# Kernel optimization log

Measured on AMD Instinct MI355X. Metric: run time of the kernel, lower is better.

## Reference

```python
import jax, jax.numpy as jnp
import numpy as np

LN_EPS = 1e-5


def conv2d(x, w, b, stride, pad):
    # x: NCHW, w: OIHW
    y = jax.lax.conv_general_dilated(
        x, w, (stride, stride), [(pad, pad), (pad, pad)],
        dimension_numbers=("NCHW", "OIHW", "NCHW"))
    return y + b[None, :, None, None]


def gdn(x, gamma, beta):
    # y_c = x_c / sqrt(beta_c + sum_j gamma_cj * x_j^2)  (1x1 conv on x^2)
    norm = jnp.einsum("bchw,dc->bdhw", x * x, gamma) + beta[None, :, None, None]
    return x / jnp.sqrt(norm)


def layernorm(x, w, b):
    mu = jnp.mean(x, axis=-1, keepdims=True)
    var = jnp.var(x, axis=-1, keepdims=True)
    return (x - mu) / jnp.sqrt(var + LN_EPS) * w + b


def setup_inputs() -> dict:
    key = jax.random.key(0)
    ks = jax.random.split(key, 16)
    r = lambda i, shape: (jax.random.normal(ks[i], shape) * 0.02).astype(jnp.float32)
    N, M, K, D = 128, 192, 192, 128
    return {
        "x_p": jax.random.normal(ks[0], (4, 16, 3, 64, 64), jnp.float32),
        "y_g": jax.random.normal(ks[1], (64, K, 32), jnp.float32),
        "conv1_w": r(2, (N, 3, 5, 5)), "conv1_b": jnp.zeros((N,), jnp.float32),
        "gamma1": (0.1 * jnp.eye(N) + 1e-3).astype(jnp.float32), "beta1": jnp.ones((N,), jnp.float32),
        "conv2_w": r(3, (N, N, 5, 5)), "conv2_b": jnp.zeros((N,), jnp.float32),
        "gamma2": (0.1 * jnp.eye(N) + 1e-3).astype(jnp.float32), "beta2": jnp.ones((N,), jnp.float32),
        "conv3_w": r(4, (M, N, 3, 3)), "conv3_b": jnp.zeros((M,), jnp.float32),
        "ln_q_w": jnp.ones((M,), jnp.float32), "ln_q_b": jnp.zeros((M,), jnp.float32),
        "ln_kv_w": jnp.ones((K,), jnp.float32), "ln_kv_b": jnp.zeros((K,), jnp.float32),
        "ln_out_w": jnp.ones((M,), jnp.float32), "ln_out_b": jnp.zeros((M,), jnp.float32),
        "Wq": r(5, (D, M)), "Wk": r(6, (D, K)), "v_w": r(7, (1, D)),
        "Wv": r(8, (M, K)), "out_w": r(9, (M, M)), "out_b": jnp.zeros((M,), jnp.float32),
    }


def reference(x_p, y_g, conv1_w, conv1_b, gamma1, beta1, conv2_w, conv2_b,
              gamma2, beta2, conv3_w, conv3_b, ln_q_w, ln_q_b, ln_kv_w, ln_kv_b,
              ln_out_w, ln_out_b, Wq, Wk, v_w, Wv, out_w, out_b):
    B, P, C, Hp, Wp = x_p.shape
    x = x_p.reshape(B * P, C, Hp, Wp)
    # local encoder: conv s2 -> GDN -> conv s2 -> GDN -> conv s1 k3
    x = gdn(conv2d(x, conv1_w, conv1_b, 2, 2), gamma1, beta1)
    x = gdn(conv2d(x, conv2_w, conv2_b, 2, 2), gamma2, beta2)
    y_local = conv2d(x, conv3_w, conv3_b, 1, 1)          # (BP, M, h, w)
    BP, M, h, w = y_local.shape
    q = y_local.reshape(BP, M, h * w).transpose(0, 2, 1)  # (BP, Tq, M)
    kv = y_g.reshape(BP, y_g.shape[1], -1).transpose(0, 2, 1)  # (BP, Tk, K)
    q = layernorm(q, ln_q_w, ln_q_b)
    kv = layernorm(kv, ln_kv_w, ln_kv_b)
    # Bahdanau additive attention
    q_proj = jnp.einsum("bqm,dm->bqd", q, Wq)            # (BP, Tq, D)
    k_proj = jnp.einsum("bkc,dc->bkd", kv, Wk)           # (BP, Tk, D)
    energy = jnp.einsum("bqkd,d->bqk",
                        jnp.tanh(q_proj[:, :, None, :] + k_proj[:, None, :, :]),
                        v_w[0])                           # (BP, Tq, Tk)
    alpha = jax.nn.softmax(energy, axis=-1)
    v_proj = jnp.einsum("bkc,mc->bkm", kv, Wv)           # (BP, Tk, M)
    context = jnp.einsum("bqk,bkm->bqm", alpha, v_proj)
    context = jnp.einsum("bqm,nm->bqn", context, out_w) + out_b
    fused = layernorm(q + context, ln_out_w, ln_out_b)
    return fused.transpose(0, 2, 1).reshape(BP, M, h, w)
```

## Files before the change

kernel.cpp:

```cpp
#include <hip/hip_runtime.h>
#include <cstddef>
#include <cstdint>


typedef __bf16 bf16x8 __attribute__((ext_vector_type(8)));
typedef float floatx4 __attribute__((ext_vector_type(4)));
typedef unsigned short ushortT;
typedef unsigned short ushort8v __attribute__((ext_vector_type(8)));

#if __has_builtin(__builtin_amdgcn_exp2f)
#define EXP2F(x) __builtin_amdgcn_exp2f(x)
#else
#define EXP2F(x) exp2f(x)
#endif
#if __has_builtin(__builtin_amdgcn_rcpf)
#define RCPF(x) __builtin_amdgcn_rcpf(x)
#else
#define RCPF(x) (1.f / (x))
#endif

__device__ __forceinline__ ushortT f2bf(float f) {
  unsigned u = __builtin_bit_cast(unsigned, f);
  unsigned r = (u + 0x7FFFu + ((u >> 16) & 1u)) >> 16;
  return (ushortT)r;
}
__device__ __forceinline__ float bf2f(ushortT u) {
  return __builtin_bit_cast(float, ((unsigned)u) << 16);
}

static constexpr size_t OFF_X2BF = 4194304;
static constexpr size_t OFF_X3BF = 9437184;
static constexpr size_t OFF_QRAW = 10485760;
static constexpr size_t OFF_WBQ  = 21299200;
static constexpr size_t OFF_WBK  = 21311488;
static constexpr size_t OFF_WBV  = 21323776;
static constexpr size_t OFF_WBO  = 21342208;
static constexpr size_t OFF_WT2  = 26079232;
static constexpr size_t OFF_WT3  = 26284032;
static constexpr size_t OFF_WC1  = 26394624;
static constexpr size_t OFF_GB1  = 26406912;
static constexpr size_t OFF_GB2  = 26415104;
static constexpr size_t OFF_KP   = 0;
static constexpr size_t OFF_VT   = 262144;

__device__ __constant__ int d_TWI2[4][9] = {{ 0, 2, 4,10,12,14,20,22,24},
                                            { 1, 3,11,13,21,23, 0, 0, 0},
                                            { 5, 7, 9,15,17,19, 0, 0, 0},
                                            { 6, 8,16,18, 0, 0, 0, 0, 0}};
__device__ __constant__ int d_NT2[4] = {9, 6, 6, 4};

__device__ void dev_convw3(const float* w, ushortT* wt, int mode, int total,
                           int idx) {
  if (idx >= total) return;
  int j    = idx & 7;
  int om   = (idx >> 3) & 63;
  int kg   = (idx >> 9) & 3;
  int slab = idx >> 11;
  int mt, s, tap, T;
  if (mode == 0) {
    int ph;
    if (slab < 72) ph = 0; else if (slab < 120) ph = 1;
    else if (slab < 168) ph = 2; else ph = 3;
    const int st[4] = {0, 72, 120, 168};
    const int ns[4] = {36, 24, 24, 16};
    int rel = slab - st[ph];
    mt = rel / ns[ph]; s = rel % ns[ph];
    tap = d_TWI2[ph][s >> 2]; T = 25;
  } else {
    mt = slab / 36; s = slab % 36; tap = s >> 2; T = 9;
  }
  int cc = s & 3;
  int c  = cc * 32 + kg * 8 + j;
  int oc = mt * 64 + om;
  wt[idx] = f2bf(w[(size_t)(oc * 128 + c) * T + tap]);
}

__device__ void dev_convw1(const float* w, ushortT* wt, int idx) {
  if (idx >= 20480) return;
  int k    = idx & 31;
  int oc   = (idx >> 5) & 127;
  int slab = idx >> 12;
  int ph, i;
  if (slab < 2) { ph = 0; i = slab; } else { ph = slab - 1; i = 0; }
  int kg = k >> 3, jj = k & 7;
  int tidx = i * 8 + jj;
  float val = 0.f;
  if (kg < 3 && tidx < d_NT2[ph]) {
    int tap = d_TWI2[ph][tidx];
    val = w[(size_t)(oc * 3 + kg) * 25 + tap];
  }
  wt[idx] = f2bf(val);
}

__device__ void dev_wcast(const float* w, ushortT* wb, int total, float scale,
                          int idx) {
  if (idx < total) wb[idx] = f2bf(w[idx] * scale);
}

__global__ __launch_bounds__(256) void prep_kernel(
    const float* __restrict__ conv2_w, ushortT* __restrict__ wt2,
    const float* __restrict__ conv3_w, ushortT* __restrict__ wt3,
    const float* __restrict__ conv1_w, ushortT* __restrict__ wc1,
    const float* __restrict__ Wq, ushortT* __restrict__ wbq,
    const float* __restrict__ Wk, ushortT* __restrict__ wbk,
    const float* __restrict__ Wv, ushortT* __restrict__ wbv,
    const float* __restrict__ out_w, ushortT* __restrict__ wbo,
    const float* __restrict__ gamma1, ushortT* __restrict__ gb1,
    const float* __restrict__ gamma2, ushortT* __restrict__ gb2) {
  constexpr float C2LE = 2.88539008177792681f;
  int blk = blockIdx.x, tid = threadIdx.x;
  if (blk < 1600)      dev_convw3(conv2_w, wt2, 0, 409600, blk * 256 + tid);
  else if (blk < 2464) dev_convw3(conv3_w, wt3, 1, 221184, (blk - 1600) * 256 + tid);
  else if (blk < 2544) dev_convw1(conv1_w, wc1, (blk - 2464) * 256 + tid);
  else if (blk < 2640) dev_wcast(Wq, wbq, 24576, C2LE, (blk - 2544) * 256 + tid);
  else if (blk < 2736) dev_wcast(Wk, wbk, 24576, C2LE, (blk - 2640) * 256 + tid);
  else if (blk < 2880) dev_wcast(Wv, wbv, 36864, 1.f, (blk - 2736) * 256 + tid);
  else if (blk < 3024) dev_wcast(out_w, wbo, 36864, 1.f, (blk - 2880) * 256 + tid);
  else if (blk < 3088) dev_wcast(gamma1, gb1, 16384, 1.f, (blk - 3024) * 256 + tid);
  else                 dev_wcast(gamma2, gb2, 16384, 1.f, (blk - 3088) * 256 + tid);
}

__global__ __launch_bounds__(256, 1) void conv1_gdn_kernel(
    const float* __restrict__ x, const ushortT* __restrict__ wc1,
    const float* __restrict__ bias, const ushortT* __restrict__ gb1,
    const float* __restrict__ beta1, ushortT* __restrict__ outb) {
  int b  = blockIdx.x >> 2;
  int yg = blockIdx.x & 3;
  int y0 = yg * 8;

  int wave = threadIdx.x >> 6;
  int lane = threadIdx.x & 63;
  int ln15 = lane & 15;
  int kg   = lane >> 4;
  int tid  = threadIdx.x;

  __shared__ ushortT smem[30280];
  ushortT* simg = smem;
  ushortT* sA   = smem + 4680;

  for (int j = tid; j < 2340; j += 256) ((unsigned*)simg)[j] = 0u;
  __syncthreads();

  int ihBase = 2 * y0 - 2;
  const float* xb = x + (size_t)b * 3 * 4096;
  for (int j = tid; j < 960; j += 256) {
    int q = j & 15;
    int rr = j >> 4;
    int c = rr / 20, ihl = rr % 20;
    int ih = ihBase + ihl;
    if (ih >= 0 && ih < 64) {
      float4 v = *(const float4*)&xb[c * 4096 + ih * 64 + q * 4];
      int pr = ih & 1, u = ih >> 1;
      int lr = u - y0 + 1;
      int base0 = ((pr * 2 + 0) * 3 + c) * 360 + lr * 36;
      int base1 = ((pr * 2 + 1) * 3 + c) * 360 + lr * 36;
      simg[base0 + 2 * q + 1] = f2bf(v.x);
      simg[base1 + 2 * q + 1] = f2bf(v.y);
      simg[base0 + 2 * q + 2] = f2bf(v.z);
      simg[base1 + 2 * q + 2] = f2bf(v.w);
    }
  }
  for (int j = tid; j < 2560; j += 256) {
    int chunk = j & 3, row = j >> 2;
    uint4 v = *(const uint4*)&wc1[row * 32 + chunk * 8];
    *(uint4*)&sA[row * 40 + chunk * 8] = v;
  }
  __syncthreads();

  constexpr int TDR[4][9] = {{-1,-1,-1, 0, 0, 0, 1, 1, 1},
                             {-1,-1, 0, 0, 1, 1, 0, 0, 0},
                             {-1,-1,-1, 0, 0, 0, 0, 0, 0},
                             {-1,-1, 0, 0, 0, 0, 0, 0, 0}};
  constexpr int TDC[4][9] = {{-1, 0, 1,-1, 0, 1,-1, 0, 1},
                             {-1, 0,-1, 0,-1, 0, 0, 0, 0},
                             {-1, 0, 1,-1, 0, 1, 0, 0, 0},
                             {-1, 0,-1, 0, 0, 0, 0, 0, 0}};
  constexpr int NT[4]  = {9, 6, 6, 4};
  constexpr int NM[4]  = {2, 1, 1, 1};
  constexpr int SB[4]  = {0, 2, 3, 4};

  ushort8v Bf[4][5];
  #pragma unroll
  for (int ntl = 0; ntl < 4; ++ntl) {
    int ntg = wave * 4 + ntl;
    int yloc = ntg >> 1;
    int xx = (ntg & 1) * 16 + ln15;
    int lbase = (yloc + 1) * 36 + xx + 1 + kg * 360;
    #pragma unroll
    for (int ph = 0; ph < 4; ++ph) {
      int pbase = ph * 1080 + lbase;
      #pragma unroll
      for (int i = 0; i < 2; ++i) {
        if (i < NM[ph]) {
          ushort8v bv;
          #pragma unroll
          for (int j = 0; j < 8; ++j) {
            int tidx = i * 8 + j;
            if (tidx >= NT[ph]) tidx = 0;
            int off = TDR[ph][tidx] * 36 + TDC[ph][tidx];
            bv[j] = simg[pbase + off];
          }
          Bf[ntl][SB[ph] + i] = bv;
        }
      }
    }
  }

  ushort4 xq[8][4];
  #pragma unroll
  for (int m = 0; m < 8; ++m) {
    bf16x8 Af[5];
    #pragma unroll
    for (int s = 0; s < 5; ++s)
      Af[s] = *(const bf16x8*)&sA[(s * 128 + m * 16 + ln15) * 40 + kg * 8];
    int oc0 = m * 16 + kg * 4;
    float4 bv = *(const float4*)&bias[oc0];
    #pragma unroll
    for (int ntl = 0; ntl < 4; ++ntl) {
      floatx4 acc = (floatx4)0.f;
      #pragma unroll
      for (int s = 0; s < 5; ++s)
        acc = __builtin_amdgcn_mfma_f32_16x16x32_bf16(
            Af[s], __builtin_bit_cast(bf16x8, Bf[ntl][s]), acc, 0, 0, 0);
      ushort4 o4 = {f2bf(acc[0] + bv.x), f2bf(acc[1] + bv.y),
                    f2bf(acc[2] + bv.z), f2bf(acc[3] + bv.w)};
      xq[m][ntl] = o4;
    }
  }
  __syncthreads();

  for (int j = tid; j < 2048; j += 256) {
    int row = j >> 4, ch = j & 15;
    *(uint4*)&smem[row * 136 + ch * 8] = *(const uint4*)&gb1[row * 128 + ch * 8];
  }
  __syncthreads();

  const int sxbase = 17408 + wave * 2176;
  #pragma unroll
  for (int q = 0; q < 4; ++q) {
    #pragma unroll
    for (int m = 0; m < 8; ++m) {
      ushort4 xv = xq[m][q];
      float f0 = bf2f(xv.x), f1 = bf2f(xv.y), f2 = bf2f(xv.z), f3 = bf2f(xv.w);
      ushort4 s4 = {f2bf(f0 * f0), f2bf(f1 * f1), f2bf(f2 * f2), f2bf(f3 * f3)};
      *(ushort4*)&smem[sxbase + ln15 * 136 + m * 16 + kg * 4] = s4;
    }
    __syncthreads();
    int ntg = wave * 4 + q;
    int y = y0 + (ntg >> 1);
    int xx = (ntg & 1) * 16 + ln15;
    int ph = ((y & 1) << 1) | (xx & 1);
    size_t dstbase = (((size_t)b * 4 + ph) * 256 + (y >> 1) * 16 + (xx >> 1)) * 128;
    #pragma unroll
    for (int dt = 0; dt < 8; ++dt) {
      floatx4 acc = (floatx4)0.f;
      #pragma unroll
      for (int k0 = 0; k0 < 4; ++k0) {
        bf16x8 ga = *(const bf16x8*)&smem[(dt * 16 + ln15) * 136 + k0 * 32 + kg * 8];
        bf16x8 xbv = *(const bf16x8*)&smem[sxbase + ln15 * 136 + k0 * 32 + kg * 8];
        acc = __builtin_amdgcn_mfma_f32_16x16x32_bf16(ga, xbv, acc, 0, 0, 0);
      }
      int d0 = dt * 16 + kg * 4;
      float4 bt = *(const float4*)&beta1[d0];
      ushort4 xv = xq[dt][q];
      ushort4 o4;
      o4.x = f2bf(bf2f(xv.x) * rsqrtf(acc[0] + bt.x));
      o4.y = f2bf(bf2f(xv.y) * rsqrtf(acc[1] + bt.y));
      o4.z = f2bf(bf2f(xv.z) * rsqrtf(acc[2] + bt.z));
      o4.w = f2bf(bf2f(xv.w) * rsqrtf(acc[3] + bt.w));
      *(ushort4*)&outb[dstbase + d0] = o4;
    }
    __syncthreads();
  }
}

__global__ __launch_bounds__(256, 2) void conv2_gdn_kernel(
    const ushortT* __restrict__ X, const ushortT* __restrict__ Wt,
    const float* __restrict__ bias, const ushortT* __restrict__ gb2,
    const float* __restrict__ beta2, ushortT* __restrict__ outb) {
  int b  = blockIdx.x >> 3;
  int rs = blockIdx.x & 7;
  int r0 = rs * 2;

  int wave = threadIdx.x >> 6;
  int lane = threadIdx.x & 63;
  int ln15 = lane & 15;
  int kg   = lane >> 4;
  int wrow  = wave & 1;
  int whalf = wave >> 1;

  __shared__ ushortT smem[31552];
  ushortT* simg = smem;
  ushortT* sGam = smem + 9792;
  ushortT* sX2  = smem + 27200;

  for (int j = threadIdx.x; j < 2048; j += 256) {
    int row = j >> 4, ch = j & 15;
    *(uint4*)&sGam[row * 136 + ch * 8] = *(const uint4*)&gb2[row * 128 + ch * 8];
  }

  floatx4 acc[4];
  #pragma unroll
  for (int m = 0; m < 4; ++m) acc[m] = (floatx4)0.f;

  constexpr int NS2[4]      = {36, 24, 24, 16};
  constexpr int PHSTART2[4] = {0, 72, 120, 168};
  constexpr int TDR_2[4][9] = {{-1,-1,-1, 0, 0, 0, 1, 1, 1},
                               {-1,-1, 0, 0, 1, 1, 0, 0, 0},
                               {-1,-1,-1, 0, 0, 0, 0, 0, 0},
                               {-1,-1, 0, 0, 0, 0, 0, 0, 0}};
  constexpr int TDC_2[4][9] = {{-1, 0, 1,-1, 0, 1,-1, 0, 1},
                               {-1, 0,-1, 0,-1, 0, 0, 0, 0},
                               {-1, 0, 1,-1, 0, 1, 0, 0, 0},
                               {-1, 0,-1, 0, 0, 0, 0, 0, 0}};

  const int aoff = kg * 512 + ln15 * 8;
  uint4 apf[8][4];

  #pragma unroll
  for (int ph = 0; ph < 4; ++ph) {
    const int NS = NS2[ph];
    const ushortT* wp0 = Wt + (size_t)(PHSTART2[ph] + whalf * NS) * 2048 + aoff;

    __syncthreads();
    const ushortT* Xb = X + (((size_t)b * 4 + ph) * 256) * 128;
    for (int idx = threadIdx.x; idx < 1152; idx += 256) {
      int chunk = idx & 15;
      int pix = idx >> 4;
      int row = pix / 18, colm = pix - row * 18;
      int i = r0 - 1 + row, j = colm - 1;
      uint4 v = {0u, 0u, 0u, 0u};
      if (i >= 0 && i < 16 && j >= 0 && j < 16)
        v = *(const uint4*)(Xb + ((size_t)(i * 16 + j)) * 128 + chunk * 8);
      *(uint4*)&simg[(row * 18 + colm) * 136 + chunk * 8] = v;
    }
    #pragma unroll
    for (int jj = 0; jj < 8; ++jj) {
      #pragma unroll
      for (int m = 0; m < 4; ++m)
        apf[jj][m] = *(const uint4*)(wp0 + (size_t)jj * 2048 + m * 128);
    }
    __syncthreads();

    #pragma unroll
    for (int s0 = 0; s0 < NS; s0 += 8) {
      #pragma unroll
      for (int jj = 0; jj < 8; ++jj) {
        int s = s0 + jj;
        if (s < NS) {
          bf16x8 acur[4];
          #pragma unroll
          for (int m = 0; m < 4; ++m) acur[m] = __builtin_bit_cast(bf16x8, apf[jj][m]);
          int sp = s + 8;
          if (sp < NS) {
            #pragma unroll
            for (int m = 0; m < 4; ++m)
              apf[jj][m] = *(const uint4*)(wp0 + (size_t)sp * 2048 + m * 128);
          }
          int t  = s >> 2;
          int c0 = (s & 3) * 32;
          int dr = TDR_2[ph][t];
          int dc = TDC_2[ph][t];
          int lrow = wrow + dr + 1;
          int lcol = ln15 + dc + 1;
          bf16x8 bfr = *(const bf16x8*)&simg[(lrow * 18 + lcol) * 136 + c0 + kg * 8];
          #pragma unroll
          for (int m = 0; m < 4; ++m)
            acc[m] = __builtin_amdgcn_mfma_f32_16x16x32_bf16(acur[m], bfr, acc[m], 0, 0, 0);
        }
      }
    }
  }

  ushort4 xq2[4];
  #pragma unroll
  for (int m = 0; m < 4; ++m) {
    int mg = whalf * 64 + m * 16 + kg * 4;
    float4 bv = *(const float4*)&bias[mg];
    ushort4 o4 = {f2bf(acc[m][0] + bv.x), f2bf(acc[m][1] + bv.y),
                  f2bf(acc[m][2] + bv.z), f2bf(acc[m][3] + bv.w)};
    xq2[m] = o4;
    float f0 = bf2f(o4.x), f1 = bf2f(o4.y), f2 = bf2f(o4.z), f3 = bf2f(o4.w);
    ushort4 s4 = {f2bf(f0 * f0), f2bf(f1 * f1), f2bf(f2 * f2), f2bf(f3 * f3)};
    *(ushort4*)&sX2[(wrow * 16 + ln15) * 136 + mg] = s4;
  }
  __syncthreads();

  int p = (r0 + wrow) * 16 + ln15;
  size_t obase = ((size_t)b * 256 + p) * 128;
  #pragma unroll
  for (int dti = 0; dti < 4; ++dti) {
    int dt = whalf * 4 + dti;
    floatx4 nacc = (floatx4)0.f;
    #pragma unroll
    for (int k0 = 0; k0 < 4; ++k0) {
      bf16x8 ga = *(const bf16x8*)&sGam[(dt * 16 + ln15) * 136 + k0 * 32 + kg * 8];
      bf16x8 xbv = *(const bf16x8*)&sX2[(wrow * 16 + ln15) * 136 + k0 * 32 + kg * 8];
      nacc = __builtin_amdgcn_mfma_f32_16x16x32_bf16(ga, xbv, nacc, 0, 0, 0);
    }
    int d0 = dt * 16 + kg * 4;
    float4 bt = *(const float4*)&beta2[d0];
    ushort4 xv = xq2[dti];
    ushort4 o4;
    o4.x = f2bf(bf2f(xv.x) * rsqrtf(nacc[0] + bt.x));
    o4.y = f2bf(bf2f(xv.y) * rsqrtf(nacc[1] + bt.y));
    o4.z = f2bf(bf2f(xv.z) * rsqrtf(nacc[2] + bt.z));
    o4.w = f2bf(bf2f(xv.w) * rsqrtf(nacc[3] + bt.w));
    *(ushort4*)&outb[obase + d0] = o4;
  }
}

__global__ __launch_bounds__(256, 2) void conv3_mfma_kernel(
    const ushortT* __restrict__ X,
    const ushortT* __restrict__ Wt,
    const float* __restrict__ bias,
    ushortT* __restrict__ outb) {
  constexpr int OC  = 192;
  constexpr int NMT = 3;

  int b   = blockIdx.x / (NMT * 4);
  int rem = blockIdx.x % (NMT * 4);
  int mt  = rem >> 2;
  int rs  = rem & 3;
  int r0  = rs * 4;

  int wave = threadIdx.x >> 6;
  int lane = threadIdx.x & 63;
  int ln15 = lane & 15;
  int kg   = lane >> 4;

  __shared__ ushortT simg[6 * 18 * 136];

  floatx4 acc[4];
  #pragma unroll
  for (int m = 0; m < 4; ++m) acc[m] = (floatx4)0.f;

  constexpr int TDR_3[9] = {-1,-1,-1, 0, 0, 0, 1, 1, 1};
  constexpr int TDC_3[9] = {-1, 0, 1,-1, 0, 1,-1, 0, 1};

  const int aoff = kg * 512 + ln15 * 8;
  uint4 apf[8][4];

  {
    const int NS = 36;
    const ushortT* wp0 = Wt + (size_t)(mt * 36) * 2048 + aoff;

    const ushortT* Xb = X + ((size_t)b * 256) * 128;
    for (int idx = threadIdx.x; idx < 1728; idx += 256) {
      int chunk = idx & 15;
      int pix = idx >> 4;
      int row = pix / 18, colm = pix - row * 18;
      int i = r0 - 1 + row, j = colm - 1;
      uint4 v = {0u, 0u, 0u, 0u};
      if (i >= 0 && i < 16 && j >= 0 && j < 16)
        v = *(const uint4*)(Xb + ((size_t)(i * 16 + j)) * 128 + chunk * 8);
      *(uint4*)&simg[(row * 18 + colm) * 136 + chunk * 8] = v;
    }
    #pragma unroll
    for (int jj = 0; jj < 8; ++jj) {
      #pragma unroll
      for (int m = 0; m < 4; ++m)
        apf[jj][m] = *(const uint4*)(wp0 + (size_t)jj * 2048 + m * 128);
    }
    __syncthreads();

    #pragma unroll
    for (int s0 = 0; s0 < NS; s0 += 8) {
      #pragma unroll
      for (int jj = 0; jj < 8; ++jj) {
        int s = s0 + jj;
        if (s < NS) {
          bf16x8 acur[4];
          #pragma unroll
          for (int m = 0; m < 4; ++m) acur[m] = __builtin_bit_cast(bf16x8, apf[jj][m]);
          int sp = s + 8;
          if (sp < NS) {
            #pragma unroll
            for (int m = 0; m < 4; ++m)
              apf[jj][m] = *(const uint4*)(wp0 + (size_t)sp * 2048 + m * 128);
          }
          int t  = s >> 2;
          int c0 = (s & 3) * 32;
          int lrow = wave + TDR_3[t] + 1;
          int lcol = ln15 + TDC_3[t] + 1;
          bf16x8 bfr = *(const bf16x8*)&simg[(lrow * 18 + lcol) * 136 + c0 + kg * 8];
          #pragma unroll
          for (int m = 0; m < 4; ++m)
            acc[m] = __builtin_amdgcn_mfma_f32_16x16x32_bf16(acur[m], bfr, acc[m], 0, 0, 0);
        }
      }
    }
  }

  #pragma unroll
  for (int m = 0; m < 4; ++m) {
    int mg = mt * 64 + m * 16 + kg * 4;
    float4 bv = *(const float4*)&bias[mg];
    int r = r0 + wave;
    int p = r * 16 + ln15;
    ushort4 o4 = {f2bf(acc[m][0] + bv.x), f2bf(acc[m][1] + bv.y),
                  f2bf(acc[m][2] + bv.z), f2bf(acc[m][3] + bv.w)};
    *(ushort4*)&outb[((size_t)b * 256 + p) * OC + mg] = o4;
  }
}

__global__ __launch_bounds__(256) void kv_prep_kernel(
    const float* __restrict__ yg, const float* __restrict__ ln_kv_w,
    const float* __restrict__ ln_kv_b, const ushortT* __restrict__ wbk,
    const ushortT* __restrict__ wbv, float* __restrict__ kp,
    ushortT* __restrict__ vT) {
  __shared__ float skvRaw[32 * 194];
  __shared__ ushortT skv[32 * 200];
  int b = blockIdx.x;
  int tid = threadIdx.x;
  int wave = tid >> 6, lane = tid & 63, ln15 = lane & 15, kg = lane >> 4;

  const float4* yg4 = (const float4*)(yg + (size_t)b * 6144);
  for (int j = tid; j < 1536; j += 256) {
    float4 v = yg4[j];
    int c = j >> 3;
    int t4 = (j & 7) * 4;
    skvRaw[(t4 + 0) * 194 + c] = v.x;
    skvRaw[(t4 + 1) * 194 + c] = v.y;
    skvRaw[(t4 + 2) * 194 + c] = v.z;
    skvRaw[(t4 + 3) * 194 + c] = v.w;
  }
  __syncthreads();
  for (int r = wave; r < 32; r += 4) {
    const float* src = skvRaw + r * 194;
    float v0 = src[lane], v1 = src[lane + 64], v2 = src[lane + 128];
    float s = v0 + v1 + v2;
    float s2 = v0 * v0 + v1 * v1 + v2 * v2;
    #pragma unroll
    for (int off = 32; off; off >>= 1) { s += __shfl_xor(s, off); s2 += __shfl_xor(s2, off); }
    float mean = s * (1.f / 192.f);
    float var = s2 * (1.f / 192.f) - mean * mean;
    float inv = rsqrtf(var + 1e-5f);
    skv[r * 200 + lane]       = f2bf((v0 - mean) * inv * ln_kv_w[lane]       + ln_kv_b[lane]);
    skv[r * 200 + lane + 64]  = f2bf((v1 - mean) * inv * ln_kv_w[lane + 64]  + ln_kv_b[lane + 64]);
    skv[r * 200 + lane + 128] = f2bf((v2 - mean) * inv * ln_kv_w[lane + 128] + ln_kv_b[lane + 128]);
  }
  __syncthreads();
  for (int ti = wave; ti < 40; ti += 4) {
    floatx4 acc = (floatx4)0.f;
    if (ti < 16) {
      int rt = ti >> 3, ct = ti & 7;
      #pragma unroll
      for (int k0 = 0; k0 < 192; k0 += 32) {
        bf16x8 afr = *(const bf16x8*)&skv[(rt * 16 + ln15) * 200 + k0 + kg * 8];
        bf16x8 bfr = *(const bf16x8*)&wbk[((size_t)(ct * 16 + ln15)) * 192 + k0 + kg * 8];
        acc = __builtin_amdgcn_mfma_f32_16x16x32_bf16(afr, bfr, acc, 0, 0, 0);
      }
      #pragma unroll
      for (int r = 0; r < 4; ++r)
        kp[((size_t)b * 32 + rt * 16 + kg * 4 + r) * 128 + ct * 16 + ln15] = acc[r];
    } else {
      int t2 = ti - 16;
      int rt = t2 / 12, ct = t2 % 12;
      #pragma unroll
      for (int k0 = 0; k0 < 192; k0 += 32) {
        bf16x8 afr = *(const bf16x8*)&skv[(rt * 16 + ln15) * 200 + k0 + kg * 8];
        bf16x8 bfr = *(const bf16x8*)&wbv[((size_t)(ct * 16 + ln15)) * 192 + k0 + kg * 8];
        acc = __builtin_amdgcn_mfma_f32_16x16x32_bf16(afr, bfr, acc, 0, 0, 0);
      }
      #pragma unroll
      for (int r = 0; r < 4; ++r)
        vT[((size_t)b * 192 + ct * 16 + ln15) * 32 + rt * 16 + kg * 4 + r] = f2bf(acc[r]);
    }
  }
}

__global__ __launch_bounds__(256) void attn_kernel(
    const ushortT* __restrict__ qrawb, const float* __restrict__ ln_q_w,
    const float* __restrict__ ln_q_b, const float* __restrict__ kp,
    const ushortT* __restrict__ vT, const ushortT* __restrict__ wbq,
    const ushortT* __restrict__ wbo, const float* __restrict__ vw,
    const float* __restrict__ out_b, const float* __restrict__ ln_out_w,
    const float* __restrict__ ln_out_b, float* __restrict__ out) {
  __shared__ ushortT smem[17284];
  ushortT* sqln = smem;
  float*   skp  = (float*)(smem + 3200);
  float*   sqpF = (float*)(smem + 11648);
  float*   se   = (float*)(smem + 15872);
  float*   swm  = (float*)(smem + 17024);
  float*   sS0  = (float*)(smem + 17280);
  ushortT* sctx = smem;
  float*   sf   = (float*)(smem + 3200);

  int b  = blockIdx.x >> 4;
  int t0 = (blockIdx.x & 15) * 16;
  int tid  = threadIdx.x;
  int wave = tid >> 6;
  int lane = tid & 63;
  int ln15 = lane & 15;
  int kg   = lane >> 4;

  {
    const float4* kp4 = (const float4*)(kp + (size_t)b * 4096);
    for (int j = tid; j < 1024; j += 256) {
      int row = j >> 5, c4 = j & 31;
      *(float4*)&skp[row * 132 + c4 * 4] = kp4[j];
    }
  }
  for (int r = wave; r < 16; r += 4) {
    const ushortT* xr = qrawb + ((size_t)(b * 256 + t0 + r)) * 192;
    float v0 = bf2f(xr[lane]), v1 = bf2f(xr[lane + 64]), v2 = bf2f(xr[lane + 128]);
    float s = v0 + v1 + v2;
    float s2 = v0 * v0 + v1 * v1 + v2 * v2;
    #pragma unroll
    for (int off = 32; off; off >>= 1) { s += __shfl_xor(s, off); s2 += __shfl_xor(s2, off); }
    float mean = s * (1.f / 192.f);
    float var = s2 * (1.f / 192.f) - mean * mean;
    float inv = rsqrtf(var + 1e-5f);
    sqln[r * 200 + lane]       = f2bf((v0 - mean) * inv * ln_q_w[lane]       + ln_q_b[lane]);
    sqln[r * 200 + lane + 64]  = f2bf((v1 - mean) * inv * ln_q_w[lane + 64]  + ln_q_b[lane + 64]);
    sqln[r * 200 + lane + 128] = f2bf((v2 - mean) * inv * ln_q_w[lane + 128] + ln_q_b[lane + 128]);
  }
  if (tid < 128) swm[tid] = -2.f * vw[tid];
  if (tid >= 128 && tid < 192) {
    int l = tid - 128;
    float s = vw[l] + vw[l + 64];
    #pragma unroll
    for (int off = 32; off; off >>= 1) s += __shfl_xor(s, off);
    if (l == 0) *sS0 = s;
  }
  __syncthreads();

  for (int ti = wave; ti < 8; ti += 4) {
    floatx4 acc = (floatx4)0.f;
    #pragma unroll
    for (int k0 = 0; k0 < 192; k0 += 32) {
      bf16x8 afr = *(const bf16x8*)&sqln[ln15 * 200 + k0 + kg * 8];
      bf16x8 bfr = *(const bf16x8*)&wbq[((size_t)(ti * 16 + ln15)) * 192 + k0 + kg * 8];
      acc = __builtin_amdgcn_mfma_f32_16x16x32_bf16(afr, bfr, acc, 0, 0, 0);
    }
    #pragma unroll
    for (int r = 0; r < 4; ++r)
      sqpF[(kg * 4 + r) * 132 + ti * 16 + ln15] = acc[r];
  }
  __syncthreads();

  {
    float S0v = *sS0;
    int qq = tid >> 4, kc = tid & 15;
    const float4* w4 = (const float4*)swm;
    const float4* q4 = (const float4*)&sqpF[qq * 132];
    const float4* ka = (const float4*)&skp[kc * 132];
    const float4* kb = (const float4*)&skp[(kc + 16) * 132];
    float acc0 = S0v, acc1 = S0v;
    #pragma unroll 8
    for (int d4 = 0; d4 < 32; ++d4) {
      float4 qv = q4[d4], k0v = ka[d4], k1v = kb[d4], wv = w4[d4];
      acc0 += wv.x * RCPF(EXP2F(qv.x + k0v.x) + 1.f);
      acc0 += wv.y * RCPF(EXP2F(qv.y + k0v.y) + 1.f);
      acc0 += wv.z * RCPF(EXP2F(qv.z + k0v.z) + 1.f);
      acc0 += wv.w * RCPF(EXP2F(qv.w + k0v.w) + 1.f);
      acc1 += wv.x * RCPF(EXP2F(qv.x + k1v.x) + 1.f);
      acc1 += wv.y * RCPF(EXP2F(qv.y + k1v.y) + 1.f);
      acc1 += wv.z * RCPF(EXP2F(qv.z + k1v.z) + 1.f);
      acc1 += wv.w * RCPF(EXP2F(qv.w + k1v.w) + 1.f);
    }
    float mx = fmaxf(acc0, acc1);
    #pragma unroll
    for (int off = 8; off; off >>= 1) mx = fmaxf(mx, __shfl_xor(mx, off));
    float e0 = __expf(acc0 - mx), e1 = __expf(acc1 - mx);
    float s = e0 + e1;
    #pragma unroll
    for (int off = 8; off; off >>= 1) s += __shfl_xor(s, off);
    float inv = 1.f / s;
    se[qq * 36 + kc]      = e0 * inv;
    se[qq * 36 + kc + 16] = e1 * inv;
  }
  __syncthreads();

  {
    float4 a0 = *(const float4*)&se[ln15 * 36 + kg * 8];
    float4 a1 = *(const float4*)&se[ln15 * 36 + kg * 8 + 4];
    ushort8v au;
    au[0] = f2bf(a0.x); au[1] = f2bf(a0.y); au[2] = f2bf(a0.z); au[3] = f2bf(a0.w);
    au[4] = f2bf(a1.x); au[5] = f2bf(a1.y); au[6] = f2bf(a1.z); au[7] = f2bf(a1.w);
    for (int ti = wave; ti < 12; ti += 4) {
      bf16x8 bfr = *(const bf16x8*)&vT[((size_t)(b * 192 + ti * 16 + ln15)) * 32 + kg * 8];
      floatx4 acc = __builtin_amdgcn_mfma_f32_16x16x32_bf16(
          __builtin_bit_cast(bf16x8, au), bfr, (floatx4)0.f, 0, 0, 0);
      #pragma unroll
      for (int r = 0; r < 4; ++r)
        sctx[(kg * 4 + r) * 200 + ti * 16 + ln15] = f2bf(acc[r]);
    }
  }
  __syncthreads();

  for (int ti = wave; ti < 12; ti += 4) {
    floatx4 acc = (floatx4)0.f;
    #pragma unroll
    for (int k0 = 0; k0 < 192; k0 += 32) {
      bf16x8 afr = *(const bf16x8*)&sctx[ln15 * 200 + k0 + kg * 8];
      bf16x8 bfr = *(const bf16x8*)&wbo[((size_t)(ti * 16 + ln15)) * 192 + k0 + kg * 8];
      acc = __builtin_amdgcn_mfma_f32_16x16x32_bf16(afr, bfr, acc, 0, 0, 0);
    }
    float bv = out_b[ti * 16 + ln15];
    #pragma unroll
    for (int r = 0; r < 4; ++r)
      sf[(kg * 4 + r) * 193 + ti * 16 + ln15] = acc[r] + bv;
  }
  __syncthreads();

  for (int rr = wave; rr < 16; rr += 4) {
    int t = t0 + rr;
    const ushortT* xr = qrawb + ((size_t)(b * 256 + t)) * 192;
    float r0_ = bf2f(xr[lane]), r1_ = bf2f(xr[lane + 64]), r2_ = bf2f(xr[lane + 128]);
    float s = r0_ + r1_ + r2_;
    float s2 = r0_ * r0_ + r1_ * r1_ + r2_ * r2_;
    #pragma unroll
    for (int off = 32; off; off >>= 1) { s += __shfl_xor(s, off); s2 += __shfl_xor(s2, off); }
    float mean = s * (1.f / 192.f);
    float var = s2 * (1.f / 192.f) - mean * mean;
    float inv = rsqrtf(var + 1e-5f);
    float q0 = (r0_ - mean) * inv * ln_q_w[lane]       + ln_q_b[lane];
    float q1 = (r1_ - mean) * inv * ln_q_w[lane + 64]  + ln_q_b[lane + 64];
    float q2 = (r2_ - mean) * inv * ln_q_w[lane + 128] + ln_q_b[lane + 128];
    float v0 = sf[rr * 193 + lane]       + q0;
    float v1 = sf[rr * 193 + lane + 64]  + q1;
    float v2 = sf[rr * 193 + lane + 128] + q2;
    float t_s = v0 + v1 + v2;
    float t_s2 = v0 * v0 + v1 * v1 + v2 * v2;
    #pragma unroll
    for (int off = 32; off; off >>= 1) { t_s += __shfl_xor(t_s, off); t_s2 += __shfl_xor(t_s2, off); }
    float m2 = t_s * (1.f / 192.f);
    float var2 = t_s2 * (1.f / 192.f) - m2 * m2;
    float inv2 = rsqrtf(var2 + 1e-5f);
    sf[rr * 193 + lane]       = (v0 - m2) * inv2 * ln_out_w[lane]       + ln_out_b[lane];
    sf[rr * 193 + lane + 64]  = (v1 - m2) * inv2 * ln_out_w[lane + 64]  + ln_out_b[lane + 64];
    sf[rr * 193 + lane + 128] = (v2 - m2) * inv2 * ln_out_w[lane + 128] + ln_out_b[lane + 128];
  }
  __syncthreads();

  for (int j = tid; j < 768; j += 256) {
    int m = j >> 2, t4 = j & 3;
    float4 o4;
    o4.x = sf[(t4 * 4 + 0) * 193 + m];
    o4.y = sf[(t4 * 4 + 1) * 193 + m];
    o4.z = sf[(t4 * 4 + 2) * 193 + m];
    o4.w = sf[(t4 * 4 + 3) * 193 + m];
    *(float4*)&out[((size_t)(b * 192 + m)) * 256 + t0 + t4 * 4] = o4;
  }
}

extern "C" void kernel_launch(void* const* d_in, const int* in_sizes, int n_in,
                              void* d_out, int out_size, void* d_ws, size_t ws_size,
                              hipStream_t stream) {
  (void)in_sizes; (void)n_in; (void)out_size; (void)ws_size;
  const float* x_p     = (const float*)d_in[0];
  const float* y_g     = (const float*)d_in[1];
  const float* conv1_w = (const float*)d_in[2];
  const float* conv1_b = (const float*)d_in[3];
  const float* gamma1  = (const float*)d_in[4];
  const float* beta1   = (const float*)d_in[5];
  const float* conv2_w = (const float*)d_in[6];
  const float* conv2_b = (const float*)d_in[7];
  const float* gamma2  = (const float*)d_in[8];
  const float* beta2   = (const float*)d_in[9];
  const float* conv3_w = (const float*)d_in[10];
  const float* conv3_b = (const float*)d_in[11];
  const float* ln_q_w  = (const float*)d_in[12];
  const float* ln_q_b  = (const float*)d_in[13];
  const float* ln_kv_w = (const float*)d_in[14];
  const float* ln_kv_b = (const float*)d_in[15];
  const float* ln_out_w= (const float*)d_in[16];
  const float* ln_out_b= (const float*)d_in[17];
  const float* Wq      = (const float*)d_in[18];
  const float* Wk      = (const float*)d_in[19];
  const float* v_w     = (const float*)d_in[20];
  const float* Wv      = (const float*)d_in[21];
  const float* out_w   = (const float*)d_in[22];
  const float* out_b   = (const float*)d_in[23];
  float* out = (float*)d_out;
  float* ws  = (float*)d_ws;

  ushortT* x2bf  = (ushortT*)(ws + OFF_X2BF);
  ushortT* x3bf  = (ushortT*)(ws + OFF_X3BF);
  ushortT* qrawb = (ushortT*)(ws + OFF_QRAW);
  ushortT* wbq   = (ushortT*)(ws + OFF_WBQ);
  ushortT* wbk   = (ushortT*)(ws + OFF_WBK);
  ushortT* wbv   = (ushortT*)(ws + OFF_WBV);
  ushortT* wbo   = (ushortT*)(ws + OFF_WBO);
  ushortT* wt2   = (ushortT*)(ws + OFF_WT2);
  ushortT* wt3   = (ushortT*)(ws + OFF_WT3);
  ushortT* wc1   = (ushortT*)(ws + OFF_WC1);
  ushortT* gb1   = (ushortT*)(ws + OFF_GB1);
  ushortT* gb2   = (ushortT*)(ws + OFF_GB2);
  float*   kp    = (float*)(ws + OFF_KP);
  ushortT* vTb   = (ushortT*)(ws + OFF_VT);

  prep_kernel<<<3152, 256, 0, stream>>>(conv2_w, wt2, conv3_w, wt3, conv1_w, wc1,
                                        Wq, wbq, Wk, wbk, Wv, wbv, out_w, wbo,
                                        gamma1, gb1, gamma2, gb2);
  kv_prep_kernel<<<64, 256, 0, stream>>>(y_g, ln_kv_w, ln_kv_b, wbk, wbv,
                                         kp, vTb);
  conv1_gdn_kernel<<<256, 256, 0, stream>>>(x_p, wc1, conv1_b, gb1, beta1, x2bf);
  conv2_gdn_kernel<<<512, 256, 0, stream>>>(x2bf, wt2, conv2_b, gb2, beta2, x3bf);
  conv3_mfma_kernel<<<768, 256, 0, stream>>>(x3bf, wt3, conv3_b, qrawb);
  attn_kernel<<<1024, 256, 0, stream>>>(qrawb, ln_q_w, ln_q_b, kp, vTb,
                                        wbq, wbo, v_w, out_b, ln_out_w,
                                        ln_out_b, out);
}
```

Measured before the change: 227.1 us.

## Retile conv1/conv2 GDN kernels and cache LN-q values in attention registers

Conv1+GDN now gives each block 4 output rows instead of 8, doubling the grid and halving per-wave tiles. It also drops the per-tile block barriers, since each wave works in its own scratch region. Conv2+GDN moves to 512-thread blocks covering 4 rows and reads gamma straight from global memory instead of staging it in shared memory. The attention kernel keeps the layer-normalised q in registers, so the final residual layernorm no longer reloads and renormalises the raw q rows, and it adds an occupancy hint. These changes trade register pressure and halo reuse for parallelism and fewer redundant loads. Gamma loads in conv2 may now hit cache instead of shared memory.

```diff
diff --git a/kernel.cpp b/kernel.cpp
--- a/kernel.cpp
+++ b/kernel.cpp
@@ -120,13 +120,13 @@
   else                 dev_wcast(gamma2, gb2, 16384, 1.f, (blk - 3088) * 256 + tid);
 }
 
-__global__ __launch_bounds__(256, 1) void conv1_gdn_kernel(
+__global__ __launch_bounds__(256, 2) void conv1_gdn_kernel(
     const float* __restrict__ x, const ushortT* __restrict__ wc1,
     const float* __restrict__ bias, const ushortT* __restrict__ gb1,
     const float* __restrict__ beta1, ushortT* __restrict__ outb) {
-  int b  = blockIdx.x >> 2;
-  int yg = blockIdx.x & 3;
-  int y0 = yg * 8;
+  int b  = blockIdx.x >> 3;
+  int yg = blockIdx.x & 7;
+  int y0 = yg * 4;
 
   int wave = threadIdx.x >> 6;
   int lane = threadIdx.x & 63;
@@ -134,26 +134,26 @@
   int kg   = lane >> 4;
   int tid  = threadIdx.x;
 
-  __shared__ ushortT smem[30280];
+  __shared__ ushortT smem[28416];
   ushortT* simg = smem;
-  ushortT* sA   = smem + 4680;
-
-  for (int j = tid; j < 2340; j += 256) ((unsigned*)simg)[j] = 0u;
+  ushortT* sA   = smem + 2816;
+
+  for (int j = tid; j < 1408; j += 256) ((unsigned*)simg)[j] = 0u;
   __syncthreads();
 
   int ihBase = 2 * y0 - 2;
   const float* xb = x + (size_t)b * 3 * 4096;
-  for (int j = tid; j < 960; j += 256) {
+  for (int j = tid; j < 576; j += 256) {
     int q = j & 15;
     int rr = j >> 4;
-    int c = rr / 20, ihl = rr % 20;
+    int c = rr / 12, ihl = rr % 12;
     int ih = ihBase + ihl;
     if (ih >= 0 && ih < 64) {
       float4 v = *(const float4*)&xb[c * 4096 + ih * 64 + q * 4];
       int pr = ih & 1, u = ih >> 1;
       int lr = u - y0 + 1;
-      int base0 = ((pr * 2 + 0) * 3 + c) * 360 + lr * 36;
-      int base1 = ((pr * 2 + 1) * 3 + c) * 360 + lr * 36;
+      int base0 = ((pr * 2 + 0) * 3 + c) * 216 + lr * 36;
+      int base1 = ((pr * 2 + 1) * 3 + c) * 216 + lr * 36;
       simg[base0 + 2 * q + 1] = f2bf(v.x);
       simg[base1 + 2 * q + 1] = f2bf(v.y);
       simg[base0 + 2 * q + 2] = f2bf(v.z);
@@ -179,16 +179,16 @@
   constexpr int NM[4]  = {2, 1, 1, 1};
   constexpr int SB[4]  = {0, 2, 3, 4};
 
-  ushort8v Bf[4][5];
-  #pragma unroll
-  for (int ntl = 0; ntl < 4; ++ntl) {
-    int ntg = wave * 4 + ntl;
+  ushort8v Bf[2][5];
+  #pragma unroll
+  for (int ntl = 0; ntl < 2; ++ntl) {
+    int ntg = wave * 2 + ntl;
     int yloc = ntg >> 1;
     int xx = (ntg & 1) * 16 + ln15;
-    int lbase = (yloc + 1) * 36 + xx + 1 + kg * 360;
+    int lbase = (yloc + 1) * 36 + xx + 1 + kg * 216;
     #pragma unroll
     for (int ph = 0; ph < 4; ++ph) {
-      int pbase = ph * 1080 + lbase;
+      int pbase = ph * 648 + lbase;
       #pragma unroll
       for (int i = 0; i < 2; ++i) {
         if (i < NM[ph]) {
@@ -206,7 +206,7 @@
     }
   }
 
-  ushort4 xq[8][4];
+  ushort4 xq[8][2];
   #pragma unroll
   for (int m = 0; m < 8; ++m) {
     bf16x8 Af[5];
@@ -216,7 +216,7 @@
     int oc0 = m * 16 + kg * 4;
     float4 bv = *(const float4*)&bias[oc0];
     #pragma unroll
-    for (int ntl = 0; ntl < 4; ++ntl) {
+    for (int ntl = 0; ntl < 2; ++ntl) {
       floatx4 acc = (floatx4)0.f;
       #pragma unroll
       for (int s = 0; s < 5; ++s)
@@ -237,7 +237,7 @@
 
   const int sxbase = 17408 + wave * 2176;
   #pragma unroll
-  for (int q = 0; q < 4; ++q) {
+  for (int q = 0; q < 2; ++q) {
     #pragma unroll
     for (int m = 0; m < 8; ++m) {
       ushort4 xv = xq[m][q];
@@ -245,8 +245,7 @@
       ushort4 s4 = {f2bf(f0 * f0), f2bf(f1 * f1), f2bf(f2 * f2), f2bf(f3 * f3)};
       *(ushort4*)&smem[sxbase + ln15 * 136 + m * 16 + kg * 4] = s4;
     }
-    __syncthreads();
-    int ntg = wave * 4 + q;
+    int ntg = wave * 2 + q;
     int y = y0 + (ntg >> 1);
     int xx = (ntg & 1) * 16 + ln15;
     int ph = ((y & 1) << 1) | (xx & 1);
@@ -270,34 +269,28 @@
       o4.w = f2bf(bf2f(xv.w) * rsqrtf(acc[3] + bt.w));
       *(ushort4*)&outb[dstbase + d0] = o4;
     }
-    __syncthreads();
-  }
-}
-
-__global__ __launch_bounds__(256, 2) void conv2_gdn_kernel(
+  }
+}
+
+__global__ __launch_bounds__(512, 2) void conv2_gdn_kernel(
     const ushortT* __restrict__ X, const ushortT* __restrict__ Wt,
     const float* __restrict__ bias, const ushortT* __restrict__ gb2,
     const float* __restrict__ beta2, ushortT* __restrict__ outb) {
-  int b  = blockIdx.x >> 3;
-  int rs = blockIdx.x & 7;
-  int r0 = rs * 2;
-
-  int wave = threadIdx.x >> 6;
-  int lane = threadIdx.x & 63;
+  int b  = blockIdx.x >> 2;
+  int rs = blockIdx.x & 3;
+  int r0 = rs * 4;
+
+  int tid  = threadIdx.x;
+  int wave = tid >> 6;
+  int lane = tid & 63;
   int ln15 = lane & 15;
   int kg   = lane >> 4;
-  int wrow  = wave & 1;
-  int whalf = wave >> 1;
-
-  __shared__ ushortT smem[31552];
+  int wrow  = wave & 3;
+  int whalf = wave >> 2;
+
+  __shared__ ushortT smem[23392];
   ushortT* simg = smem;
-  ushortT* sGam = smem + 9792;
-  ushortT* sX2  = smem + 27200;
-
-  for (int j = threadIdx.x; j < 2048; j += 256) {
-    int row = j >> 4, ch = j & 15;
-    *(uint4*)&sGam[row * 136 + ch * 8] = *(const uint4*)&gb2[row * 128 + ch * 8];
-  }
+  ushortT* sX2  = smem + 14688;
 
   floatx4 acc[4];
   #pragma unroll
@@ -324,7 +317,7 @@
 
     __syncthreads();
     const ushortT* Xb = X + (((size_t)b * 4 + ph) * 256) * 128;
-    for (int idx = threadIdx.x; idx < 1152; idx += 256) {
+    for (int idx = tid; idx < 1728; idx += 512) {
       int chunk = idx & 15;
       int pix = idx >> 4;
       int row = pix / 18, colm = pix - row * 18;
@@ -394,7 +387,7 @@
     floatx4 nacc = (floatx4)0.f;
     #pragma unroll
     for (int k0 = 0; k0 < 4; ++k0) {
-      bf16x8 ga = *(const bf16x8*)&sGam[(dt * 16 + ln15) * 136 + k0 * 32 + kg * 8];
+      bf16x8 ga = *(const bf16x8*)&gb2[(size_t)(dt * 16 + ln15) * 128 + k0 * 32 + kg * 8];
       bf16x8 xbv = *(const bf16x8*)&sX2[(wrow * 16 + ln15) * 136 + k0 * 32 + kg * 8];
       nacc = __builtin_amdgcn_mfma_f32_16x16x32_bf16(ga, xbv, nacc, 0, 0, 0);
     }
@@ -570,7 +563,7 @@
   }
 }
 
-__global__ __launch_bounds__(256) void attn_kernel(
+__global__ __launch_bounds__(256, 4) void attn_kernel(
     const ushortT* __restrict__ qrawb, const float* __restrict__ ln_q_w,
     const float* __restrict__ ln_q_b, const float* __restrict__ kp,
     const ushortT* __restrict__ vT, const ushortT* __restrict__ wbq,
@@ -602,19 +595,30 @@
       *(float4*)&skp[row * 132 + c4 * 4] = kp4[j];
     }
   }
-  for (int r = wave; r < 16; r += 4) {
-    const ushortT* xr = qrawb + ((size_t)(b * 256 + t0 + r)) * 192;
-    float v0 = bf2f(xr[lane]), v1 = bf2f(xr[lane + 64]), v2 = bf2f(xr[lane + 128]);
-    float s = v0 + v1 + v2;
-    float s2 = v0 * v0 + v1 * v1 + v2 * v2;
-    #pragma unroll
-    for (int off = 32; off; off >>= 1) { s += __shfl_xor(s, off); s2 += __shfl_xor(s2, off); }
-    float mean = s * (1.f / 192.f);
-    float var = s2 * (1.f / 192.f) - mean * mean;
-    float inv = rsqrtf(var + 1e-5f);
-    sqln[r * 200 + lane]       = f2bf((v0 - mean) * inv * ln_q_w[lane]       + ln_q_b[lane]);
-    sqln[r * 200 + lane + 64]  = f2bf((v1 - mean) * inv * ln_q_w[lane + 64]  + ln_q_b[lane + 64]);
-    sqln[r * 200 + lane + 128] = f2bf((v2 - mean) * inv * ln_q_w[lane + 128] + ln_q_b[lane + 128]);
+  float qreg[4][3];
+  {
+    float w0 = ln_q_w[lane], w1 = ln_q_w[lane + 64], w2 = ln_q_w[lane + 128];
+    float b0 = ln_q_b[lane], b1 = ln_q_b[lane + 64], b2 = ln_q_b[lane + 128];
+    #pragma unroll
+    for (int i = 0; i < 4; ++i) {
+      int r = wave + i * 4;
+      const ushortT* xr = qrawb + ((size_t)(b * 256 + t0 + r)) * 192;
+      float v0 = bf2f(xr[lane]), v1 = bf2f(xr[lane + 64]), v2 = bf2f(xr[lane + 128]);
+      float s = v0 + v1 + v2;
+      float s2 = v0 * v0 + v1 * v1 + v2 * v2;
+      #pragma unroll
+      for (int off = 32; off; off >>= 1) { s += __shfl_xor(s, off); s2 += __shfl_xor(s2, off); }
+      float mean = s * (1.f / 192.f);
+      float var = s2 * (1.f / 192.f) - mean * mean;
+      float inv = rsqrtf(var + 1e-5f);
+      float q0 = (v0 - mean) * inv * w0 + b0;
+      float q1 = (v1 - mean) * inv * w1 + b1;
+      float q2 = (v2 - mean) * inv * w2 + b2;
+      qreg[i][0] = q0; qreg[i][1] = q1; qreg[i][2] = q2;
+      sqln[r * 200 + lane]       = f2bf(q0);
+      sqln[r * 200 + lane + 64]  = f2bf(q1);
+      sqln[r * 200 + lane + 128] = f2bf(q2);
+    }
   }
   if (tid < 128) swm[tid] = -2.f * vw[tid];
   if (tid >= 128 && tid < 192) {
@@ -705,23 +709,12 @@
   }
   __syncthreads();
 
-  for (int rr = wave; rr < 16; rr += 4) {
-    int t = t0 + rr;
-    const ushortT* xr = qrawb + ((size_t)(b * 256 + t)) * 192;
-    float r0_ = bf2f(xr[lane]), r1_ = bf2f(xr[lane + 64]), r2_ = bf2f(xr[lane + 128]);
-    float s = r0_ + r1_ + r2_;
-    float s2 = r0_ * r0_ + r1_ * r1_ + r2_ * r2_;
-    #pragma unroll
-    for (int off = 32; off; off >>= 1) { s += __shfl_xor(s, off); s2 += __shfl_xor(s2, off); }
-    float mean = s * (1.f / 192.f);
-    float var = s2 * (1.f / 192.f) - mean * mean;
-    float inv = rsqrtf(var + 1e-5f);
-    float q0 = (r0_ - mean) * inv * ln_q_w[lane]       + ln_q_b[lane];
-    float q1 = (r1_ - mean) * inv * ln_q_w[lane + 64]  + ln_q_b[lane + 64];
-    float q2 = (r2_ - mean) * inv * ln_q_w[lane + 128] + ln_q_b[lane + 128];
-    float v0 = sf[rr * 193 + lane]       + q0;
-    float v1 = sf[rr * 193 + lane + 64]  + q1;
-    float v2 = sf[rr * 193 + lane + 128] + q2;
+  #pragma unroll
+  for (int i = 0; i < 4; ++i) {
+    int rr = wave + i * 4;
+    float v0 = sf[rr * 193 + lane]       + qreg[i][0];
+    float v1 = sf[rr * 193 + lane + 64]  + qreg[i][1];
+    float v2 = sf[rr * 193 + lane + 128] + qreg[i][2];
     float t_s = v0 + v1 + v2;
     float t_s2 = v0 * v0 + v1 * v1 + v2 * v2;
     #pragma unroll
@@ -797,8 +790,8 @@
                                         gamma1, gb1, gamma2, gb2);
   kv_prep_kernel<<<64, 256, 0, stream>>>(y_g, ln_kv_w, ln_kv_b, wbk, wbv,
                                          kp, vTb);
-  conv1_gdn_kernel<<<256, 256, 0, stream>>>(x_p, wc1, conv1_b, gb1, beta1, x2bf);
-  conv2_gdn_kernel<<<512, 256, 0, stream>>>(x2bf, wt2, conv2_b, gb2, beta2, x3bf);
+  conv1_gdn_kernel<<<512, 256, 0, stream>>>(x_p, wc1, conv1_b, gb1, beta1, x2bf);
+  conv2_gdn_kernel<<<256, 512, 0, stream>>>(x2bf, wt2, conv2_b, gb2, beta2, x3bf);
   conv3_mfma_kernel<<<768, 256, 0, stream>>>(x3bf, wt3, conv3_b, qrawb);
   attn_kernel<<<1024, 256, 0, stream>>>(qrawb, ln_q_w, ln_q_b, kp, vTb,
                                         wbq, wbo, v_w, out_b, ln_out_w,
```

Result: faster. 219.6 us (-3.3%).
